# Performance work log

Hardware: AMD Instinct MI355X
Metric: run time of the kernel (lower is better)

Reference implementation:

```python
import jax, jax.numpy as jnp
import numpy as np

N_HEADS = 16

def _apply_rope(x, cos_pos, sin_pos):
    # x: [B,S,H,Dh]; cos_pos/sin_pos: [1,S,1,Dh//2]
    x1, x2 = jnp.split(x, 2, axis=-1)  # matches torch reshape (...,2,Dh//2) split
    x1r = x1 * cos_pos - x2 * sin_pos
    x2r = x2 * cos_pos + x1 * sin_pos
    return jnp.concatenate([x1r, x2r], axis=-1)

def setup_inputs() -> dict:
    key = jax.random.key(0)
    ks = jax.random.split(key, 8)
    B, S, D = 2, 2048, 1024
    Dh = D // N_HEADS
    hidden_states = jax.random.normal(ks[0], (B, S, D), dtype=jnp.float32)
    # rotary tables: cos/sin of theta; use realistic RoPE frequencies
    inv_freq = 1.0 / (10000.0 ** (jnp.arange(0, Dh, 2, dtype=jnp.float32) / Dh))  # [Dh//2]
    t = jnp.arange(S, dtype=jnp.float32)
    freqs = jnp.outer(t, inv_freq)  # [S, Dh//2]
    cos = jnp.cos(freqs)
    sin = jnp.sin(freqs)
    # additive causal mask [1,1,S,S]
    causal = jnp.tril(jnp.ones((S, S), dtype=bool))
    attention_mask = jnp.where(causal, 0.0, -1e9).astype(jnp.float32)[None, None]
    scale = 1.0 / np.sqrt(D)
    Wq = jax.random.normal(ks[1], (D, D), dtype=jnp.float32) * scale
    Wk = jax.random.normal(ks[2], (D, D), dtype=jnp.float32) * scale
    Wv = jax.random.normal(ks[3], (D, D), dtype=jnp.float32) * scale
    Wo = jax.random.normal(ks[4], (D, D), dtype=jnp.float32) * scale
    return {"hidden_states": hidden_states, "cos": cos, "sin": sin,
            "attention_mask": attention_mask, "Wq": Wq, "Wk": Wk, "Wv": Wv, "Wo": Wo}

def reference(hidden_states, cos, sin, attention_mask, Wq, Wk, Wv, Wo):
    B, S, D = hidden_states.shape
    H = N_HEADS
    Dh = D // H
    scaling = Dh ** -0.5
    q = (hidden_states @ Wq).reshape(B, S, H, Dh)
    k = (hidden_states @ Wk).reshape(B, S, H, Dh)
    v = (hidden_states @ Wv).reshape(B, S, H, Dh)
    cos_pos = cos[None, :, None, :]  # [1,S,1,Dh//2]
    sin_pos = sin[None, :, None, :]
    q = _apply_rope(q, cos_pos, sin_pos)
    k = _apply_rope(k, cos_pos, sin_pos)
    # eager attention: [B,H,S,S] scores
    scores = jnp.einsum('bihd,bjhd->bhij', q * scaling, k)
    scores = scores + attention_mask
    probs = jax.nn.softmax(scores, axis=-1)
    out = jnp.einsum('bhij,bjhd->bihd', probs, v).reshape(B, S, D)
    return out @ Wo
```

## Files before the change

### kernel.cpp

```cpp
#include <hip/hip_runtime.h>
#include <cstdint>
#include <cstddef>

using u16 = unsigned short;
using s16x8 = __attribute__((ext_vector_type(8))) short;
using f32x4 = __attribute__((ext_vector_type(4))) float;

#define GADDR(p) ((const __attribute__((address_space(1))) void*)(p))
#define LADDR(p) ((__attribute__((address_space(3))) void*)(p))

static constexpr int S_LEN = 2048;
static constexpr float L2E = 1.44269504088896f;

#if __has_builtin(__builtin_amdgcn_exp2f)
#define EXP2(x) __builtin_amdgcn_exp2f(x)
#else
#define EXP2(x) exp2f(x)
#endif

__device__ __forceinline__ u16 f2bf(float x) {
  union { float f; unsigned u; } v; v.f = x;
  return (u16)((v.u + 0x7FFFu + ((v.u >> 16) & 1u)) >> 16);
}
__device__ __forceinline__ float bf2f(u16 x) {
  union { unsigned u; float f; } v; v.u = (unsigned)x << 16;
  return v.f;
}
__device__ __forceinline__ unsigned pk2(float a, float b) {
#if __has_builtin(__builtin_amdgcn_perm)
  return __builtin_amdgcn_perm(__float_as_uint(b) + 0x8000u,
                               __float_as_uint(a) + 0x8000u, 0x07060302u);
#else
  union { float f; unsigned u; } x, y; x.f = a; y.f = b;
  return ((x.u + 0x8000u) >> 16) | ((y.u + 0x8000u) & 0xFFFF0000u);
#endif
}

__device__ __constant__ unsigned char T_IT[48] = {
  31,31,30,30,29,28,15,14,
  29,28,27,27,26,26,25,24,13,12,
  25,24,23,23,22,22,21,20,11,10,
  21,20,19,19,18,18,17,16,9,8,
  17,16,7,6,
  5,4, 3,2, 1,0};
__device__ __constant__ unsigned char T_C0[48] = {
  0,1,0,1,0,0,0,0,
  1,1,0,1,0,1,0,0,0,0,
  1,1,0,1,0,1,0,0,0,0,
  1,1,0,1,0,1,0,0,0,0,
  1,1,0,0,
  0,0, 0,0, 0,0};

__global__ __launch_bounds__(256) void prep_k(const float* __restrict__ X,
                                              u16* __restrict__ Xb,
                                              const float* __restrict__ Wq,
                                              const float* __restrict__ Wk,
                                              const float* __restrict__ Wv,
                                              const float* __restrict__ Wo,
                                              u16* __restrict__ WtAll) {
  const int bid = blockIdx.x, tid = threadIdx.x;
  if (bid < 4096) {
    int i = (bid * 256 + tid) * 4;
    float4 v = *(const float4*)(X + i);
    uint2 pk; pk.x = pk2(v.x, v.y); pk.y = pk2(v.z, v.w);
    *(uint2*)(Xb + i) = pk;
    return;
  }
  const int r4 = bid - 4096;
  const int z = r4 >> 8, rem = r4 & 255;
  const float* W = (z == 0) ? Wq : (z == 1) ? Wk : (z == 2) ? Wv : Wo;
  u16* Wt = WtAll + ((size_t)z << 20);
  const int k0 = (rem >> 4) * 64, n0 = (rem & 15) * 64;
  __shared__ float t[64][65];
  #pragma unroll
  for (int it = 0; it < 4; ++it) {
    int slot = it * 256 + tid;
    int r = slot >> 4, cq = slot & 15;
    float4 v = *(const float4*)&W[(size_t)(k0 + r) * 1024 + n0 + cq * 4];
    t[r][cq * 4 + 0] = v.x; t[r][cq * 4 + 1] = v.y;
    t[r][cq * 4 + 2] = v.z; t[r][cq * 4 + 3] = v.w;
  }
  __syncthreads();
  #pragma unroll
  for (int it = 0; it < 16; ++it) {
    int slot = it * 256 + tid;
    int rn = slot >> 6, ck = slot & 63;
    Wt[(size_t)(n0 + rn) * 1024 + k0 + ck] = f2bf(t[ck][rn]);
  }
}

__global__ __launch_bounds__(256, 2) void gemm_k(
    const u16* __restrict__ A, const u16* __restrict__ WtAll,
    const float* __restrict__ cosT, const float* __restrict__ sinT,
    u16* __restrict__ Qb, u16* __restrict__ Kb, u16* __restrict__ Vt,
    float* __restrict__ Of, int modeBase) {
  const int tid = threadIdx.x, lane = tid & 63, wv = tid >> 6;
  const int mode = modeBase + blockIdx.z;
  const u16* Wp = WtAll + ((size_t)mode << 20);
  const int m0 = blockIdx.x * 128, n0 = blockIdx.y * 128;
  const int wm = (wv >> 1) * 64, wn = (wv & 1) * 64;
  __shared__ __align__(16) u16 As[128 * 32];
  __shared__ __align__(16) u16 Bs[128 * 32];
  f32x4 acc[4][4];
  const f32x4 zf = {0.f, 0.f, 0.f, 0.f};
  #pragma unroll
  for (int i = 0; i < 4; ++i)
    #pragma unroll
    for (int j = 0; j < 4; ++j) acc[i][j] = zf;
  const int q = lane >> 4, l15 = lane & 15;

  for (int k0 = 0; k0 < 1024; k0 += 32) {
    __syncthreads();
    #pragma unroll
    for (int call = 0; call < 2; ++call) {
      int slot = call * 256 + tid;
      int row = slot >> 2, c = slot & 3;
      int sc = c ^ ((row >> 1) & 3);
      __builtin_amdgcn_global_load_lds(
          GADDR(A + (size_t)(m0 + row) * 1024 + k0 + sc * 8),
          LADDR(As + (size_t)(call * 256 + wv * 64) * 8), 16, 0, 0);
      __builtin_amdgcn_global_load_lds(
          GADDR(Wp + (size_t)(n0 + row) * 1024 + k0 + sc * 8),
          LADDR(Bs + (size_t)(call * 256 + wv * 64) * 8), 16, 0, 0);
    }
    __syncthreads();
    s16x8 af[4], bfr[4];
    #pragma unroll
    for (int mt = 0; mt < 4; ++mt) {
      int r = wm + mt * 16 + l15;
      af[mt] = *(const s16x8*)(As + r * 32 + ((q ^ ((r >> 1) & 3)) << 3));
    }
    #pragma unroll
    for (int nt = 0; nt < 4; ++nt) {
      int r = wn + nt * 16 + l15;
      bfr[nt] = *(const s16x8*)(Bs + r * 32 + ((q ^ ((r >> 1) & 3)) << 3));
    }
    #pragma unroll
    for (int mt = 0; mt < 4; ++mt)
      #pragma unroll
      for (int nt = 0; nt < 4; ++nt)
        acc[mt][nt] = __builtin_amdgcn_mfma_f32_16x16x32_bf16(af[mt], bfr[nt], acc[mt][nt], 0, 0, 0);
  }

  if (mode < 2) {
    u16* outP = (mode == 0) ? Qb : Kb;
    const float scl = (mode == 0) ? 0.125f * L2E : 1.0f;
    #pragma unroll
    for (int mt = 0; mt < 4; ++mt)
      #pragma unroll
      for (int rg = 0; rg < 4; ++rg) {
        int rowg = m0 + wm + mt * 16 + q * 4 + rg;
        int b = rowg >> 11, s = rowg & 2047;
        #pragma unroll
        for (int ntl = 0; ntl < 2; ++ntl) {
          int col = n0 + wn + ntl * 16 + l15;
          int h = col >> 6, dl = col & 31;
          float cc = cosT[s * 32 + dl], ss = sinT[s * 32 + dl];
          float xlo = acc[mt][ntl][rg];
          float xhi = acc[mt][ntl + 2][rg];
          size_t base = ((size_t)(b * 16 + h) * 2048 + s) * 64 + dl;
          outP[base]      = f2bf((xlo * cc - xhi * ss) * scl);
          outP[base + 32] = f2bf((xhi * cc + xlo * ss) * scl);
        }
      }
  } else if (mode == 2) {
    #pragma unroll
    for (int mt = 0; mt < 4; ++mt) {
      int rowg = m0 + wm + mt * 16 + q * 4;
      int b = rowg >> 11, s = rowg & 2047;
      #pragma unroll
      for (int nt = 0; nt < 4; ++nt) {
        int col = n0 + wn + nt * 16 + l15;
        int h = col >> 6, d = col & 63;
        uint2 pk;
        pk.x = pk2(acc[mt][nt][0], acc[mt][nt][1]);
        pk.y = pk2(acc[mt][nt][2], acc[mt][nt][3]);
        *(uint2*)(Vt + ((size_t)((b * 16 + h) * 64 + d) * 2048 + s)) = pk;
      }
    }
  } else {
    #pragma unroll
    for (int mt = 0; mt < 4; ++mt)
      #pragma unroll
      for (int rg = 0; rg < 4; ++rg) {
        int rowg = m0 + wm + mt * 16 + q * 4 + rg;
        #pragma unroll
        for (int nt = 0; nt < 4; ++nt) {
          int col = n0 + wn + nt * 16 + l15;
          Of[(size_t)rowg * 1024 + col] = acc[mt][nt][rg];
        }
      }
  }
}

__global__ __launch_bounds__(256, 3) void flash_k(
    const u16* __restrict__ Qb, const u16* __restrict__ Kb,
    const u16* __restrict__ Vt, u16* __restrict__ Aout,
    char* __restrict__ Pscr) {
  const int tid = threadIdx.x, lane = tid & 63, wv = tid >> 6;
  const int q = lane >> 4, l15 = lane & 15;
  __shared__ __align__(16) u16 Ks[128 * 64];
  __shared__ __align__(16) u16 Vs[64 * 128];
  __shared__ __align__(16) u16 Ps[4][16 * 128];
  u16* Pw = Ps[wv];
  const f32x4 zf = {0.f, 0.f, 0.f, 0.f};

  #pragma unroll 1
  for (int half = 0; half < 2; ++half) {
    const unsigned c = half ? (1535u - blockIdx.x) : blockIdx.x;
    const int bh = (int)(c & 31u), local = (int)(c >> 5);
    const int it = T_IT[local], c0 = T_C0[local];
    const int len = (it >> 1) + 1, mid = (len + 1) >> 1;
    const int jt0 = c0 ? mid : 0;
    const int jtE = (it >= 16) ? (c0 ? len : mid) : len;
    const int i0 = it * 64;
    const int iw = i0 + wv * 16 + l15;
    const u16* Qh = Qb + (size_t)bh * S_LEN * 64;
    const u16* Kh = Kb + (size_t)bh * S_LEN * 64;
    const u16* Vh = Vt + (size_t)bh * 64 * S_LEN;

    s16x8 bq[2];
    #pragma unroll
    for (int ks = 0; ks < 2; ++ks)
      bq[ks] = *(const s16x8*)(Qh + (size_t)iw * 64 + ks * 32 + q * 8);

    f32x4 O[4];
    float mst = -1e30f, lst = 0.f;
    #pragma unroll
    for (int i = 0; i < 4; ++i) O[i] = zf;

    for (int jt = jt0; jt < jtE; ++jt) {
      const int j0 = jt * 128;
      __syncthreads();
      #pragma unroll
      for (int cc = 0; cc < 4; ++cc) {
        const int wc = cc * 4 + wv;
        {
          int jr = wc * 8 + (lane >> 3);
          int u = (lane & 7) ^ (jr & 7);
          __builtin_amdgcn_global_load_lds(
              GADDR(Kh + (size_t)(j0 + jr) * 64 + u * 8),
              LADDR(Ks + wc * 512), 16, 0, 0);
        }
        {
          int d = wc * 4 + (lane >> 4);
          int uv = (lane & 15) ^ (d & 15);
          __builtin_amdgcn_global_load_lds(
              GADDR(Vh + (size_t)d * S_LEN + j0 + uv * 8),
              LADDR(Vs + wc * 512), 16, 0, 0);
        }
      }
      __syncthreads();

      f32x4 sf[8];
      #pragma unroll
      for (int j = 0; j < 8; ++j) sf[j] = zf;
      #pragma unroll
      for (int ks = 0; ks < 2; ++ks)
        #pragma unroll
        for (int mt = 0; mt < 8; ++mt) {
          int jr = mt * 16 + l15;
          int u = ((ks * 4 + q) ^ (jr & 7));
          s16x8 ak = *(const s16x8*)(Ks + jr * 64 + u * 8);
          sf[mt] = __builtin_amdgcn_mfma_f32_16x16x32_bf16(ak, bq[ks], sf[mt], 0, 0, 0);
        }

      if (jt == len - 1) {
        #pragma unroll
        for (int mt = 0; mt < 8; ++mt)
          #pragma unroll
          for (int rg = 0; rg < 4; ++rg) {
            int j = j0 + mt * 16 + q * 4 + rg;
            if (j > iw) sf[mt][rg] = -1e30f;
          }
      }

      float mx = sf[0][0];
      #pragma unroll
      for (int mt = 0; mt < 8; ++mt)
        #pragma unroll
        for (int rg = 0; rg < 4; ++rg) mx = fmaxf(mx, sf[mt][rg]);
      mx = fmaxf(mx, __shfl_xor(mx, 16, 64));
      mx = fmaxf(mx, __shfl_xor(mx, 32, 64));
      const bool nonew = __all(mx <= mst);
      float al = 1.0f;
      if (!nonew) {
        float mn = fmaxf(mst, mx);
        al = EXP2(mst - mn);
        mst = mn;
      }
      float sum = 0.f;
      #pragma unroll
      for (int mt = 0; mt < 8; ++mt) {
        float p0 = EXP2(sf[mt][0] - mst), p1 = EXP2(sf[mt][1] - mst);
        float p2 = EXP2(sf[mt][2] - mst), p3 = EXP2(sf[mt][3] - mst);
        sum += (p0 + p1) + (p2 + p3);
        uint2 pk; pk.x = pk2(p0, p1); pk.y = pk2(p2, p3);
        int cj = (mt * 4 + q) ^ l15;
        *(uint2*)(Pw + l15 * 128 + cj * 4) = pk;
      }
      sum += __shfl_xor(sum, 16, 64);
      sum += __shfl_xor(sum, 32, 64);
      if (!nonew) {
        lst = al * lst + sum;
        #pragma unroll
        for (int ntd = 0; ntd < 4; ++ntd)
          #pragma unroll
          for (int rg = 0; rg < 4; ++rg) O[ntd][rg] *= al;
      } else {
        lst += sum;
      }

      asm volatile("s_waitcnt lgkmcnt(0)" ::: "memory");

      s16x8 bp[4];
      #pragma unroll
      for (int ks = 0; ks < 4; ++ks) {
        int u0 = ks * 8 + q * 2;
        union { s16x8 v; uint2 d[2]; } f;
        f.d[0] = *(const uint2*)(Pw + l15 * 128 + ((u0) ^ l15) * 4);
        f.d[1] = *(const uint2*)(Pw + l15 * 128 + ((u0 + 1) ^ l15) * 4);
        bp[ks] = f.v;
      }
      #pragma unroll
      for (int ks = 0; ks < 4; ++ks)
        #pragma unroll
        for (int ntd = 0; ntd < 4; ++ntd) {
          int d = ntd * 16 + l15;
          int uv = (ks * 4 + q) ^ l15;
          s16x8 av = *(const s16x8*)(Vs + d * 128 + uv * 8);
          O[ntd] = __builtin_amdgcn_mfma_f32_16x16x32_bf16(av, bp[ks], O[ntd], 0, 0, 0);
        }
    }

    if (it < 16) {
      const float inv = 1.0f / lst;
      const int b = bh >> 4, h = bh & 15;
      u16* dst = Aout + ((size_t)(b * 2048 + iw)) * 1024 + h * 64;
      #pragma unroll
      for (int ntd = 0; ntd < 4; ++ntd) {
        uint2 pk;
        pk.x = pk2(O[ntd][0] * inv, O[ntd][1] * inv);
        pk.y = pk2(O[ntd][2] * inv, O[ntd][3] * inv);
        *(uint2*)(dst + ntd * 16 + q * 4) = pk;
      }
    } else {
      const int slot = (bh * 16 + (it - 16)) * 2 + c0;
      char* pb = Pscr + (size_t)slot * 8704;
      float* Pm = (float*)pb;
      u16* Po = (u16*)(pb + 512);
      const int il = wv * 16 + l15;
      if (q == 0) { Pm[il] = mst; Pm[64 + il] = lst; }
      #pragma unroll
      for (int ntd = 0; ntd < 4; ++ntd) {
        uint2 pk;
        pk.x = pk2(O[ntd][0], O[ntd][1]);
        pk.y = pk2(O[ntd][2], O[ntd][3]);
        *(uint2*)(Po + il * 64 + ntd * 16 + q * 4) = pk;
      }
    }
  }
}

__global__ __launch_bounds__(256) void combine_k(const char* __restrict__ Pscr,
                                                 u16* __restrict__ Aout) {
  const int blk = blockIdx.x;
  const int bh = blk >> 4, itm = blk & 15;
  const char* b0 = Pscr + (size_t)((bh * 16 + itm) * 2 + 0) * 8704;
  const char* b1 = Pscr + (size_t)((bh * 16 + itm) * 2 + 1) * 8704;
  const int t = threadIdx.x;
  const int r = t >> 2, dseg = (t & 3) * 16;
  const float m0 = ((const float*)b0)[r], l0 = ((const float*)b0)[64 + r];
  const float m1 = ((const float*)b1)[r], l1 = ((const float*)b1)[64 + r];
  const float M = fmaxf(m0, m1);
  const float w0 = EXP2(m0 - M), w1 = EXP2(m1 - M);
  const float inv = 1.0f / (w0 * l0 + w1 * l1);
  const u16* O0 = (const u16*)(b0 + 512) + r * 64 + dseg;
  const u16* O1 = (const u16*)(b1 + 512) + r * 64 + dseg;
  unsigned outv[8];
  #pragma unroll
  for (int v8 = 0; v8 < 2; ++v8) {
    s16x8 a = *(const s16x8*)(O0 + v8 * 8);
    s16x8 bb = *(const s16x8*)(O1 + v8 * 8);
    #pragma unroll
    for (int jp = 0; jp < 4; ++jp) {
      float e0 = (w0 * bf2f((u16)a[jp * 2])     + w1 * bf2f((u16)bb[jp * 2]))     * inv;
      float e1 = (w0 * bf2f((u16)a[jp * 2 + 1]) + w1 * bf2f((u16)bb[jp * 2 + 1])) * inv;
      outv[v8 * 4 + jp] = pk2(e0, e1);
    }
  }
  const int b = bh >> 4, h = bh & 15;
  const int s = (itm + 16) * 64 + r;
  u16* dst = Aout + ((size_t)(b * 2048 + s)) * 1024 + h * 64 + dseg;
  *(uint4*)dst = *(const uint4*)outv;
  *(uint4*)(dst + 8) = *(const uint4*)(outv + 4);
}

extern "C" void kernel_launch(void* const* d_in, const int* in_sizes, int n_in,
                              void* d_out, int out_size, void* d_ws, size_t ws_size,
                              hipStream_t stream) {
  const float* X    = (const float*)d_in[0];
  const float* cosT = (const float*)d_in[1];
  const float* sinT = (const float*)d_in[2];
  const float* Wq = (const float*)d_in[4];
  const float* Wk = (const float*)d_in[5];
  const float* Wv = (const float*)d_in[6];
  const float* Wo = (const float*)d_in[7];
  float* Of = (float*)d_out;

  u16* ws  = (u16*)d_ws;
  u16* Xb  = ws;
  u16* Wt  = ws + (4u << 20);
  u16* Qb  = ws + (8u << 20);
  u16* Kb  = ws + (12u << 20);
  u16* Vtb = ws + (20u << 20);
  char* Pscr = (char*)d_out;

  prep_k<<<5120, 256, 0, stream>>>(X, Xb, Wq, Wk, Wv, Wo, Wt);
  gemm_k<<<dim3(32, 8, 3), 256, 0, stream>>>(Xb, Wt, cosT, sinT, Qb, Kb, Vtb, nullptr, 0);
  flash_k<<<768, 256, 0, stream>>>(Qb, Kb, Vtb, Xb, Pscr);
  combine_k<<<512, 256, 0, stream>>>(Pscr, Xb);
  gemm_k<<<dim3(32, 8, 1), 256, 0, stream>>>(Xb, Wt, cosT, sinT, nullptr, nullptr, nullptr, Of, 3);
}
```

Baseline: 193.5 us.

## Prefetch next K/V tile into registers instead of direct global-to-LDS loads

```diff
diff --git a/kernel.cpp b/kernel.cpp
--- a/kernel.cpp
+++ b/kernel.cpp
@@ -205,6 +205,19 @@
   u16* Pw = Ps[wv];
   const f32x4 zf = {0.f, 0.f, 0.f, 0.f};
 
+  int kOff[4], vOff[4];
+  u16 *kDst[4], *vDst[4];
+  #pragma unroll
+  for (int cc = 0; cc < 4; ++cc) {
+    const int wc = cc * 4 + wv;
+    const int jr = wc * 8 + (lane >> 3);
+    kOff[cc] = jr * 64 + (((lane & 7) ^ (jr & 7)) << 3);
+    const int d = wc * 4 + (lane >> 4);
+    vOff[cc] = d * S_LEN + (((lane & 15) ^ (d & 15)) << 3);
+    kDst[cc] = Ks + wc * 512 + lane * 8;
+    vDst[cc] = Vs + wc * 512 + lane * 8;
+  }
+
   #pragma unroll 1
   for (int half = 0; half < 2; ++half) {
     const unsigned c = half ? (1535u - blockIdx.x) : blockIdx.x;
@@ -224,6 +237,13 @@
     for (int ks = 0; ks < 2; ++ks)
       bq[ks] = *(const s16x8*)(Qh + (size_t)iw * 64 + ks * 32 + q * 8);
 
+    s16x8 kreg[4], vreg[4];
+    #pragma unroll
+    for (int cc = 0; cc < 4; ++cc) {
+      kreg[cc] = *(const s16x8*)(Kh + (size_t)jt0 * 8192 + kOff[cc]);
+      vreg[cc] = *(const s16x8*)(Vh + (size_t)jt0 * 128 + vOff[cc]);
+    }
+
     f32x4 O[4];
     float mst = -1e30f, lst = 0.f;
     #pragma unroll
@@ -234,20 +254,15 @@
       __syncthreads();
       #pragma unroll
       for (int cc = 0; cc < 4; ++cc) {
-        const int wc = cc * 4 + wv;
-        {
-          int jr = wc * 8 + (lane >> 3);
-          int u = (lane & 7) ^ (jr & 7);
-          __builtin_amdgcn_global_load_lds(
-              GADDR(Kh + (size_t)(j0 + jr) * 64 + u * 8),
-              LADDR(Ks + wc * 512), 16, 0, 0);
-        }
-        {
-          int d = wc * 4 + (lane >> 4);
-          int uv = (lane & 15) ^ (d & 15);
-          __builtin_amdgcn_global_load_lds(
-              GADDR(Vh + (size_t)d * S_LEN + j0 + uv * 8),
-              LADDR(Vs + wc * 512), 16, 0, 0);
+        *(s16x8*)kDst[cc] = kreg[cc];
+        *(s16x8*)vDst[cc] = vreg[cc];
+      }
+      if (jt + 1 < jtE) {
+        const int jn = j0 + 128;
+        #pragma unroll
+        for (int cc = 0; cc < 4; ++cc) {
+          kreg[cc] = *(const s16x8*)(Kh + (size_t)jn * 64 + kOff[cc]);
+          vreg[cc] = *(const s16x8*)(Vh + (size_t)jn + vOff[cc]);
         }
       }
       __syncthreads();
```

Result: slower. 207.5 us (+7.2%).

## Double GEMM K-tile to 64 and add smaller-M output projection kernel

Applied to the files above, without the earlier changes.

```diff
diff --git a/kernel.cpp b/kernel.cpp
--- a/kernel.cpp
+++ b/kernel.cpp
@@ -93,14 +93,14 @@
     const u16* __restrict__ A, const u16* __restrict__ WtAll,
     const float* __restrict__ cosT, const float* __restrict__ sinT,
     u16* __restrict__ Qb, u16* __restrict__ Kb, u16* __restrict__ Vt,
-    float* __restrict__ Of, int modeBase) {
+    int modeBase) {
   const int tid = threadIdx.x, lane = tid & 63, wv = tid >> 6;
   const int mode = modeBase + blockIdx.z;
   const u16* Wp = WtAll + ((size_t)mode << 20);
   const int m0 = blockIdx.x * 128, n0 = blockIdx.y * 128;
   const int wm = (wv >> 1) * 64, wn = (wv & 1) * 64;
-  __shared__ __align__(16) u16 As[128 * 32];
-  __shared__ __align__(16) u16 Bs[128 * 32];
+  __shared__ __align__(16) u16 As[128 * 64];
+  __shared__ __align__(16) u16 Bs[128 * 64];
   f32x4 acc[4][4];
   const f32x4 zf = {0.f, 0.f, 0.f, 0.f};
   #pragma unroll
@@ -109,37 +109,42 @@
     for (int j = 0; j < 4; ++j) acc[i][j] = zf;
   const int q = lane >> 4, l15 = lane & 15;
 
-  for (int k0 = 0; k0 < 1024; k0 += 32) {
+  for (int k0 = 0; k0 < 1024; k0 += 64) {
     __syncthreads();
     #pragma unroll
-    for (int call = 0; call < 2; ++call) {
+    for (int call = 0; call < 4; ++call) {
       int slot = call * 256 + tid;
-      int row = slot >> 2, c = slot & 3;
-      int sc = c ^ ((row >> 1) & 3);
+      int row = slot >> 3, u = (slot & 7) ^ (row & 7);
       __builtin_amdgcn_global_load_lds(
-          GADDR(A + (size_t)(m0 + row) * 1024 + k0 + sc * 8),
-          LADDR(As + (size_t)(call * 256 + wv * 64) * 8), 16, 0, 0);
+          GADDR(A + (size_t)(m0 + row) * 1024 + k0 + u * 8),
+          LADDR(As + (size_t)slot * 8), 16, 0, 0);
       __builtin_amdgcn_global_load_lds(
-          GADDR(Wp + (size_t)(n0 + row) * 1024 + k0 + sc * 8),
-          LADDR(Bs + (size_t)(call * 256 + wv * 64) * 8), 16, 0, 0);
+          GADDR(Wp + (size_t)(n0 + row) * 1024 + k0 + u * 8),
+          LADDR(Bs + (size_t)slot * 8), 16, 0, 0);
     }
     __syncthreads();
-    s16x8 af[4], bfr[4];
+    s16x8 af[4][2], bfr[4][2];
     #pragma unroll
     for (int mt = 0; mt < 4; ++mt) {
       int r = wm + mt * 16 + l15;
-      af[mt] = *(const s16x8*)(As + r * 32 + ((q ^ ((r >> 1) & 3)) << 3));
+      #pragma unroll
+      for (int ks = 0; ks < 2; ++ks)
+        af[mt][ks] = *(const s16x8*)(As + r * 64 + (((ks * 4 + q) ^ (r & 7)) << 3));
     }
     #pragma unroll
     for (int nt = 0; nt < 4; ++nt) {
       int r = wn + nt * 16 + l15;
-      bfr[nt] = *(const s16x8*)(Bs + r * 32 + ((q ^ ((r >> 1) & 3)) << 3));
-    }
-    #pragma unroll
-    for (int mt = 0; mt < 4; ++mt)
-      #pragma unroll
-      for (int nt = 0; nt < 4; ++nt)
-        acc[mt][nt] = __builtin_amdgcn_mfma_f32_16x16x32_bf16(af[mt], bfr[nt], acc[mt][nt], 0, 0, 0);
+      #pragma unroll
+      for (int ks = 0; ks < 2; ++ks)
+        bfr[nt][ks] = *(const s16x8*)(Bs + r * 64 + (((ks * 4 + q) ^ (r & 7)) << 3));
+    }
+    #pragma unroll
+    for (int ks = 0; ks < 2; ++ks)
+      #pragma unroll
+      for (int mt = 0; mt < 4; ++mt)
+        #pragma unroll
+        for (int nt = 0; nt < 4; ++nt)
+          acc[mt][nt] = __builtin_amdgcn_mfma_f32_16x16x32_bf16(af[mt][ks], bfr[nt][ks], acc[mt][nt], 0, 0, 0);
   }
 
   if (mode < 2) {
@@ -163,7 +168,7 @@
           outP[base + 32] = f2bf((xhi * cc + xlo * ss) * scl);
         }
       }
-  } else if (mode == 2) {
+  } else {
     #pragma unroll
     for (int mt = 0; mt < 4; ++mt) {
       int rowg = m0 + wm + mt * 16 + q * 4;
@@ -178,19 +183,80 @@
         *(uint2*)(Vt + ((size_t)((b * 16 + h) * 64 + d) * 2048 + s)) = pk;
       }
     }
-  } else {
-    #pragma unroll
-    for (int mt = 0; mt < 4; ++mt)
-      #pragma unroll
-      for (int rg = 0; rg < 4; ++rg) {
-        int rowg = m0 + wm + mt * 16 + q * 4 + rg;
-        #pragma unroll
-        for (int nt = 0; nt < 4; ++nt) {
-          int col = n0 + wn + nt * 16 + l15;
-          Of[(size_t)rowg * 1024 + col] = acc[mt][nt][rg];
-        }
-      }
-  }
+  }
+}
+
+__global__ __launch_bounds__(256, 2) void gemmo_k(
+    const u16* __restrict__ A, const u16* __restrict__ WtAll,
+    float* __restrict__ Of) {
+  const int tid = threadIdx.x, lane = tid & 63, wv = tid >> 6;
+  const u16* Wp = WtAll + ((size_t)3 << 20);
+  const int m0 = blockIdx.x * 64, n0 = blockIdx.y * 128;
+  const int wm = (wv >> 1) * 32, wn = (wv & 1) * 64;
+  __shared__ __align__(16) u16 As[64 * 64];
+  __shared__ __align__(16) u16 Bs[128 * 64];
+  f32x4 acc[2][4];
+  const f32x4 zf = {0.f, 0.f, 0.f, 0.f};
+  #pragma unroll
+  for (int i = 0; i < 2; ++i)
+    #pragma unroll
+    for (int j = 0; j < 4; ++j) acc[i][j] = zf;
+  const int q = lane >> 4, l15 = lane & 15;
+
+  for (int k0 = 0; k0 < 1024; k0 += 64) {
+    __syncthreads();
+    #pragma unroll
+    for (int call = 0; call < 2; ++call) {
+      int slot = call * 256 + tid;
+      int row = slot >> 3, u = (slot & 7) ^ (row & 7);
+      __builtin_amdgcn_global_load_lds(
+          GADDR(A + (size_t)(m0 + row) * 1024 + k0 + u * 8),
+          LADDR(As + (size_t)slot * 8), 16, 0, 0);
+    }
+    #pragma unroll
+    for (int call = 0; call < 4; ++call) {
+      int slot = call * 256 + tid;
+      int row = slot >> 3, u = (slot & 7) ^ (row & 7);
+      __builtin_amdgcn_global_load_lds(
+          GADDR(Wp + (size_t)(n0 + row) * 1024 + k0 + u * 8),
+          LADDR(Bs + (size_t)slot * 8), 16, 0, 0);
+    }
+    __syncthreads();
+    s16x8 af[2][2], bfr[4][2];
+    #pragma unroll
+    for (int mt = 0; mt < 2; ++mt) {
+      int r = wm + mt * 16 + l15;
+      #pragma unroll
+      for (int ks = 0; ks < 2; ++ks)
+        af[mt][ks] = *(const s16x8*)(As + r * 64 + (((ks * 4 + q) ^ (r & 7)) << 3));
+    }
+    #pragma unroll
+    for (int nt = 0; nt < 4; ++nt) {
+      int r = wn + nt * 16 + l15;
+      #pragma unroll
+      for (int ks = 0; ks < 2; ++ks)
+        bfr[nt][ks] = *(const s16x8*)(Bs + r * 64 + (((ks * 4 + q) ^ (r & 7)) << 3));
+    }
+    #pragma unroll
+    for (int ks = 0; ks < 2; ++ks)
+      #pragma unroll
+      for (int mt = 0; mt < 2; ++mt)
+        #pragma unroll
+        for (int nt = 0; nt < 4; ++nt)
+          acc[mt][nt] = __builtin_amdgcn_mfma_f32_16x16x32_bf16(af[mt][ks], bfr[nt][ks], acc[mt][nt], 0, 0, 0);
+  }
+
+  #pragma unroll
+  for (int mt = 0; mt < 2; ++mt)
+    #pragma unroll
+    for (int rg = 0; rg < 4; ++rg) {
+      int rowg = m0 + wm + mt * 16 + q * 4 + rg;
+      #pragma unroll
+      for (int nt = 0; nt < 4; ++nt) {
+        int col = n0 + wn + nt * 16 + l15;
+        Of[(size_t)rowg * 1024 + col] = acc[mt][nt][rg];
+      }
+    }
 }
 
 __global__ __launch_bounds__(256, 3) void flash_k(
@@ -417,8 +483,8 @@
   char* Pscr = (char*)d_out;
 
   prep_k<<<5120, 256, 0, stream>>>(X, Xb, Wq, Wk, Wv, Wo, Wt);
-  gemm_k<<<dim3(32, 8, 3), 256, 0, stream>>>(Xb, Wt, cosT, sinT, Qb, Kb, Vtb, nullptr, 0);
+  gemm_k<<<dim3(32, 8, 3), 256, 0, stream>>>(Xb, Wt, cosT, sinT, Qb, Kb, Vtb, 0);
   flash_k<<<768, 256, 0, stream>>>(Qb, Kb, Vtb, Xb, Pscr);
   combine_k<<<512, 256, 0, stream>>>(Pscr, Xb);
-  gemm_k<<<dim3(32, 8, 1), 256, 0, stream>>>(Xb, Wt, cosT, sinT, nullptr, nullptr, nullptr, Of, 3);
-}
+  gemmo_k<<<dim3(64, 8), 256, 0, stream>>>(Xb, Wt, Of);
+}
```

New measurement: 186.4 us. 1.04x faster.
